# Kernel tuning notes

Measured on AMD Instinct MI355X. Metric: run time of the kernel, lower is better.

Reference implementation:

```python
import jax, jax.numpy as jnp
import numpy as np

N = 50000        # num nodes
E = 1_000_000    # num edges
F_IN = 256       # input feature dim
UNITS = 128      # hidden units
NUM_CLASSES = 40 # output classes
EPS = 1e-3       # Keras BatchNormalization default epsilon


def setup_inputs() -> dict:
    key = jax.random.key(0)
    ks = jax.random.split(key, 32)
    inp = {
        "x": jax.random.normal(ks[0], (N, F_IN), jnp.float32),
        "edge_index": jax.random.randint(ks[1], (2, E), 0, N, jnp.int32),
        "edge_weight": jax.random.uniform(ks[2], (E,), jnp.float32),
    }
    dims = [(F_IN, UNITS), (UNITS, UNITS), (UNITS, NUM_CLASSES)]
    ki = 3
    for li, (fi, fo) in enumerate(dims, 1):
        inp[f"w_gcn{li}"] = jax.random.normal(ks[ki], (fi, fo), jnp.float32) / np.sqrt(fi).astype(np.float32); ki += 1
        inp[f"w_self{li}"] = jax.random.normal(ks[ki], (fi, fo), jnp.float32) / np.sqrt(fi).astype(np.float32); ki += 1
        inp[f"b{li}"] = jnp.zeros((fo,), jnp.float32)
        inp[f"gamma{li}"] = 1.0 + 0.1 * jax.random.normal(ks[ki], (fo,), jnp.float32); ki += 1
        inp[f"beta{li}"] = 0.1 * jax.random.normal(ks[ki], (fo,), jnp.float32); ki += 1
        inp[f"mean{li}"] = 0.1 * jax.random.normal(ks[ki], (fo,), jnp.float32); ki += 1
        inp[f"var{li}"] = jnp.ones((fo,), jnp.float32)
    return inp


def _gcn_bs(h, src, dst, norm_w, w_gcn, w_self, b, gamma, beta, mean, var, act):
    # GCN aggregation: transform then gather->weight->scatter-sum
    hw = h @ w_gcn                                   # [N, out]
    msg = hw[src] * norm_w[:, None]                  # [E, out]
    agg = jax.ops.segment_sum(msg, dst, num_segments=N)
    out = agg + h @ w_self + b                       # self-loop dense + bias
    # BatchNorm (inference: moving stats)
    out = (out - mean) * jax.lax.rsqrt(var + EPS) * gamma + beta
    return act(out) if act is not None else out


def reference(x, edge_index, edge_weight,
              w_gcn1, w_self1, b1, gamma1, beta1, mean1, var1,
              w_gcn2, w_self2, b2, gamma2, beta2, mean2, var2,
              w_gcn3, w_self3, b3, gamma3, beta3, mean3, var3):
    src, dst = edge_index[0], edge_index[1]
    # symmetric GCN normalization (renorm=False: no added self loops)
    deg = jax.ops.segment_sum(edge_weight, dst, num_segments=N)
    dinv = jnp.where(deg > 0, jax.lax.rsqrt(jnp.where(deg > 0, deg, 1.0)), 0.0)
    norm_w = dinv[src] * edge_weight * dinv[dst]
    # inference: DropEdge and Dropout are identity
    h = _gcn_bs(x, src, dst, norm_w, w_gcn1, w_self1, b1, gamma1, beta1, mean1, var1, jax.nn.relu)
    h = _gcn_bs(h, src, dst, norm_w, w_gcn2, w_self2, b2, gamma2, beta2, mean2, var2, jax.nn.relu)
    h = _gcn_bs(h, src, dst, norm_w, w_gcn3, w_self3, b3, gamma3, beta3, mean3, var3, None)
    return h
```

## Files before the change

kernel.cpp:

```cpp
#include <hip/hip_runtime.h>
#include <hip/hip_bf16.h>

#define NN 50000
#define EE 1000000
static constexpr float EPSV = 1e-3f;
static constexpr float FIXSCALE = 16777216.f;

typedef __attribute__((ext_vector_type(8))) short short8;
typedef __attribute__((ext_vector_type(4))) float fx4;

__device__ inline float blo(unsigned u) { return __uint_as_float(u << 16); }
__device__ inline float bhi(unsigned u) { return __uint_as_float(u & 0xffff0000u); }
__device__ inline unsigned short f2b(float f) {
    __hip_bfloat16 h = __float2bfloat16(f);
    return *(unsigned short*)&h;
}
__device__ inline unsigned pack2(float a, float b) {
    return (unsigned)f2b(a) | ((unsigned)f2b(b) << 16);
}

__device__ inline void gload_lds16(const unsigned short* g, unsigned short* ldsbase) {
    __builtin_amdgcn_global_load_lds(
        (const __attribute__((address_space(1))) unsigned int*)(const void*)g,
        (__attribute__((address_space(3))) unsigned int*)(void*)ldsbase, 16, 0, 0);
}


#define ZB 196
#define WB1 256
#define WB2 128
#define WB3 64

__global__ void setup_kernel(unsigned long long* __restrict__ cnt64p,
                             const float* __restrict__ wg1, const float* __restrict__ ws1,
                             unsigned short* __restrict__ Wt1,
                             const float* __restrict__ wg2, const float* __restrict__ ws2,
                             unsigned short* __restrict__ Wt2,
                             const float* __restrict__ wg3, const float* __restrict__ ws3,
                             unsigned short* __restrict__ Wt3) {
    int b = blockIdx.x;
    int t = threadIdx.x;
    if (b < ZB) {
        int i = b * 256 + t;
        if (i < NN) cnt64p[(size_t)i << 3] = 0ull;
    } else if (b < ZB + WB1) {
        int idx = (b - ZB) * 256 + t;
        int n = idx >> 8, k = idx & 255;
        float v = (n < 128) ? wg1[(size_t)k * 128 + n]
                            : ws1[(size_t)k * 128 + (n - 128)];
        Wt1[idx] = f2b(v);
    } else if (b < ZB + WB1 + WB2) {
        int idx = (b - ZB - WB1) * 256 + t;
        int n = idx >> 7, k = idx & 127;
        float v = (n < 128) ? wg2[(size_t)k * 128 + n]
                            : ws2[(size_t)k * 128 + (n - 128)];
        Wt2[idx] = f2b(v);
    } else {
        int idx = (b - ZB - WB1 - WB2) * 256 + t;
        int n = idx >> 7, k = idx & 127;
        float v = 0.f;
        if (n < 40) v = wg3[(size_t)k * 40 + n];
        else if (n < 80) v = ws3[(size_t)k * 40 + (n - 40)];
        Wt3[idx] = f2b(v);
    }
}


#define CB 3907

__global__ void pre_kernel(const int* __restrict__ ei, const float* __restrict__ ew,
                           unsigned long long* __restrict__ cnt64p, unsigned* __restrict__ rank) {
    int e = blockIdx.x * 256 + threadIdx.x;
    if (e < EE) {
        int d = ei[EE + e];
        unsigned fx = __float2uint_rn(ew[e] * FIXSCALE);
        unsigned long long old =
            atomicAdd(&cnt64p[(size_t)d << 3], 0x100000000ull | (unsigned long long)fx);
        rank[e] = (unsigned)(old >> 32);
    }
}


__global__ __launch_bounds__(1024) void dinvsum_kernel(const unsigned long long* __restrict__ cnt64p,
                                                       float* __restrict__ dinv,
                                                       int* __restrict__ bsum) {
    __shared__ int s[1024];
    const int t = threadIdx.x;
    int idx = blockIdx.x * 1024 + t;
    unsigned long long cv = 0ull;
    if (idx < NN) cv = cnt64p[(size_t)idx << 3];
    float deg = (float)(unsigned)cv * (1.f / FIXSCALE);
    if (idx < NN) dinv[idx] = (deg > 0.f) ? rsqrtf(deg) : 0.f;
    s[t] = (int)(unsigned)(cv >> 32);
    __syncthreads();
#pragma unroll
    for (int off = 512; off > 0; off >>= 1) {
        if (t < off) s[t] += s[t + off];
        __syncthreads();
    }
    if (t == 0) bsum[blockIdx.x] = s[0];
}

__global__ __launch_bounds__(64) void scanB_kernel(const int* __restrict__ bsum,
                                                   int* __restrict__ bpre, int nb) {
    int t = threadIdx.x;
    int v = (t < nb) ? bsum[t] : 0;
    int own = v;
#pragma unroll
    for (int off = 1; off < 64; off <<= 1) {
        int u = __shfl_up(v, off);
        if (t >= off) v += u;
    }
    if (t < nb) bpre[t] = v - own;
}

__global__ __launch_bounds__(1024) void scanC_kernel(const unsigned long long* __restrict__ cnt64p,
                                                     const int* __restrict__ bpre,
                                                     int* __restrict__ rowstart) {
    __shared__ int s[1024];
    const int t = threadIdx.x;
    int idx = blockIdx.x * 1024 + t;
    int v = (idx < NN) ? (int)(unsigned)(cnt64p[(size_t)idx << 3] >> 32) : 0;
    s[t] = v;
    __syncthreads();
#pragma unroll
    for (int off = 1; off < 1024; off <<= 1) {
        int u = (t >= off) ? s[t - off] : 0;
        __syncthreads();
        s[t] += u;
        __syncthreads();
    }
    if (idx < NN) rowstart[idx] = s[t] - v + bpre[blockIdx.x];
    if (idx == 0) rowstart[NN] = EE;
}

__global__ void fill_kernel(const int* __restrict__ ei, const float* __restrict__ ew,
                            const float* __restrict__ dinv, const int* __restrict__ rowstart,
                            const unsigned* __restrict__ rank, unsigned* __restrict__ eprec4) {
    int e = blockIdx.x * blockDim.x + threadIdx.x;
    if (e >= EE) return;
    int s = ei[e], d = ei[EE + e];
    int idx = rowstart[d] + (int)rank[e];
    float w = dinv[s] * ew[e] * dinv[d];
    eprec4[idx] = ((unsigned)s << 16) | (unsigned)f2b(w);
}


template <bool AF32>
__global__ __launch_bounds__(256) void gemm_mfma(const void* __restrict__ Av,
                                                 const unsigned short* __restrict__ Wt,
                                                 const float* __restrict__ bias,
                                                 unsigned short* __restrict__ Cg,
                                                 unsigned short* __restrict__ Cs,
                                                 int M, int K, int Fo) {
    __shared__ unsigned short sA[64 * 64];
    __shared__ unsigned short sB[128 * 64];

    const int t = threadIdx.x;
    const int lane = t & 63;
    const int wave = t >> 6;
    const int l15 = lane & 15, quad = lane >> 4;
    const int row0 = blockIdx.x * 64;
    const int colbase = blockIdx.y * 128;

    fx4 acc[4][2];
#pragma unroll
    for (int r = 0; r < 4; ++r)
#pragma unroll
        for (int c = 0; c < 2; ++c) acc[r][c] = (fx4){0.f, 0.f, 0.f, 0.f};

    for (int kc = 0; kc < K; kc += 64) {
#pragma unroll
        for (int j = 0; j < 6; ++j) {
            int o = wave * 6 + j;
            int ak = kc + (o & 1) * 32 + quad * 8;
            if (o < 8) {
                int ar = row0 + (o >> 1) * 16 + l15;
                if (ar >= M) ar = M - 1;
                if constexpr (AF32) {
                    const float* Af = (const float*)Av;
                    const float4* p = (const float4*)(Af + (size_t)ar * K + ak);
                    float4 v0 = p[0], v1 = p[1];
                    uint4 u;
                    u.x = pack2(v0.x, v0.y);
                    u.y = pack2(v0.z, v0.w);
                    u.z = pack2(v1.x, v1.y);
                    u.w = pack2(v1.z, v1.w);
                    *reinterpret_cast<uint4*>(sA + o * 512 + lane * 8) = u;
                } else {
                    gload_lds16((const unsigned short*)Av + (size_t)ar * K + ak, sA + o * 512);
                }
            } else {
                int bo = o - 8;
                int br = colbase + (bo >> 1) * 16 + l15;
                gload_lds16(Wt + (size_t)br * K + ak, sB + bo * 512);
            }
        }
        __syncthreads();

#pragma unroll
        for (int kh = 0; kh < 2; ++kh) {
            short8 a[4], b[2];
#pragma unroll
            for (int r = 0; r < 4; ++r)
                a[r] = *reinterpret_cast<const short8*>(&sA[(r * 2 + kh) * 512 + lane * 8]);
#pragma unroll
            for (int c = 0; c < 2; ++c)
                b[c] = *reinterpret_cast<const short8*>(&sB[((wave * 2 + c) * 2 + kh) * 512 + lane * 8]);
#pragma unroll
            for (int r = 0; r < 4; ++r)
#pragma unroll
                for (int c = 0; c < 2; ++c)
                    acc[r][c] = __builtin_amdgcn_mfma_f32_16x16x32_bf16(a[r], b[c], acc[r][c], 0, 0, 0);
        }
        __syncthreads();
    }

#pragma unroll
    for (int r = 0; r < 4; ++r) {
#pragma unroll
        for (int reg = 0; reg < 4; ++reg) {
            int row = row0 + r * 16 + quad * 4 + reg;
            if (row >= M) continue;
#pragma unroll
            for (int c = 0; c < 2; ++c) {
                int f = colbase + wave * 32 + c * 16 + l15;
                if (f >= 2 * Fo) continue;
                bool isG = (f < Fo);
                int col = isG ? f : f - Fo;
                float badd = isG ? 0.f : bias[col];
                unsigned short* basep = isG ? Cg : Cs;
                basep[(size_t)row * Fo + col] = f2b(acc[r][c][reg] + badd);
            }
        }
    }
}


template <bool RELU>
__global__ __launch_bounds__(256) void agg128_kernel(
    const int* __restrict__ rowstart, const unsigned* __restrict__ eprec4,
    const unsigned* __restrict__ hw, const unsigned* __restrict__ selfC,
    const float* __restrict__ g, const float* __restrict__ be,
    const float* __restrict__ mu, const float* __restrict__ va,
    unsigned* __restrict__ out) {
    int wave = threadIdx.x >> 6;
    int lane = threadIdx.x & 63;
    int n = blockIdx.x * 4 + wave;
    if (n >= NN) return;
    unsigned scp = selfC[n * 64 + lane];
    float acc0 = blo(scp), acc1 = bhi(scp);
    int beg = rowstart[n], end = rowstart[n + 1];
    int i = beg;

    if (i + 16 <= end) {
        unsigned e[16];
        {
            int ifl = __builtin_amdgcn_readfirstlane(i);
#pragma unroll
            for (int k = 0; k < 16; ++k) e[k] = eprec4[ifl + k];
        }
        for (; i + 32 <= end; i += 16) {
            unsigned v[16];
#pragma unroll
            for (int k = 0; k < 16; ++k) v[k] = hw[(e[k] >> 16) * 64u + lane];
            unsigned en[16];
            {
                int ifl = __builtin_amdgcn_readfirstlane(i + 16);
#pragma unroll
                for (int k = 0; k < 16; ++k) en[k] = eprec4[ifl + k];
            }
#pragma unroll
            for (int k = 0; k < 16; ++k) {
                float w = blo(e[k]);
                acc0 += blo(v[k]) * w;
                acc1 += bhi(v[k]) * w;
            }
#pragma unroll
            for (int k = 0; k < 16; ++k) e[k] = en[k];
        }
        unsigned v[16];
#pragma unroll
        for (int k = 0; k < 16; ++k) v[k] = hw[(e[k] >> 16) * 64u + lane];
#pragma unroll
        for (int k = 0; k < 16; ++k) {
            float w = blo(e[k]);
            acc0 += blo(v[k]) * w;
            acc1 += bhi(v[k]) * w;
        }
        i += 16;
    }
    for (; i + 4 <= end; i += 4) {
        unsigned e0 = eprec4[i], e1 = eprec4[i + 1], e2 = eprec4[i + 2], e3 = eprec4[i + 3];
        unsigned v0 = hw[(e0 >> 16) * 64u + lane];
        unsigned v1 = hw[(e1 >> 16) * 64u + lane];
        unsigned v2 = hw[(e2 >> 16) * 64u + lane];
        unsigned v3 = hw[(e3 >> 16) * 64u + lane];
        float w0 = blo(e0), w1 = blo(e1), w2 = blo(e2), w3 = blo(e3);
        acc0 += blo(v0) * w0; acc1 += bhi(v0) * w0;
        acc0 += blo(v1) * w1; acc1 += bhi(v1) * w1;
        acc0 += blo(v2) * w2; acc1 += bhi(v2) * w2;
        acc0 += blo(v3) * w3; acc1 += bhi(v3) * w3;
    }
    for (; i < end; ++i) {
        unsigned e = eprec4[i];
        unsigned v = hw[(e >> 16) * 64u + lane];
        float w = blo(e);
        acc0 += blo(v) * w; acc1 += bhi(v) * w;
    }
    float2 m2 = reinterpret_cast<const float2*>(mu)[lane];
    float2 v2f = reinterpret_cast<const float2*>(va)[lane];
    float2 g2 = reinterpret_cast<const float2*>(g)[lane];
    float2 b2 = reinterpret_cast<const float2*>(be)[lane];
    float r0 = (acc0 - m2.x) * rsqrtf(v2f.x + EPSV) * g2.x + b2.x;
    float r1 = (acc1 - m2.y) * rsqrtf(v2f.y + EPSV) * g2.y + b2.y;
    if (RELU) {
        r0 = fmaxf(r0, 0.f);
        r1 = fmaxf(r1, 0.f);
    }
    out[n * 64 + lane] = pack2(r0, r1);
}


__global__ __launch_bounds__(256) void agg40_kernel(
    const int* __restrict__ rowstart, const unsigned* __restrict__ eprec4,
    const unsigned* __restrict__ hw, const unsigned* __restrict__ selfC,
    const float* __restrict__ g, const float* __restrict__ be,
    const float* __restrict__ mu, const float* __restrict__ va,
    float* __restrict__ out) {
    int wave = threadIdx.x >> 6;
    int lane = threadIdx.x & 63;
    int n = blockIdx.x * 4 + wave;
    if (n >= NN) return;
    int grp = lane / 20;
    int fl = lane - grp * 20;
    float acc0 = 0.f, acc1 = 0.f;
    int beg = rowstart[n], end = rowstart[n + 1];
    if (grp < 3) {
        int i = beg + grp;
        for (; i + 9 < end; i += 12) {
            unsigned e0 = eprec4[i], e1 = eprec4[i + 3], e2 = eprec4[i + 6], e3 = eprec4[i + 9];
            unsigned v0 = hw[(e0 >> 16) * 20u + fl];
            unsigned v1 = hw[(e1 >> 16) * 20u + fl];
            unsigned v2 = hw[(e2 >> 16) * 20u + fl];
            unsigned v3 = hw[(e3 >> 16) * 20u + fl];
            float w0 = blo(e0), w1 = blo(e1), w2 = blo(e2), w3 = blo(e3);
            acc0 += blo(v0) * w0; acc1 += bhi(v0) * w0;
            acc0 += blo(v1) * w1; acc1 += bhi(v1) * w1;
            acc0 += blo(v2) * w2; acc1 += bhi(v2) * w2;
            acc0 += blo(v3) * w3; acc1 += bhi(v3) * w3;
        }
        for (; i < end; i += 3) {
            unsigned e = eprec4[i];
            unsigned v = hw[(e >> 16) * 20u + fl];
            float w = blo(e);
            acc0 += blo(v) * w;
            acc1 += bhi(v) * w;
        }
    }
    acc0 += __shfl(acc0, lane + 20) + __shfl(acc0, lane + 40);
    acc1 += __shfl(acc1, lane + 20) + __shfl(acc1, lane + 40);
    if (lane < 20) {
        int f0 = lane * 2;
        unsigned scp = selfC[n * 20 + lane];
        acc0 += blo(scp);
        acc1 += bhi(scp);
        float2 m2 = reinterpret_cast<const float2*>(mu)[lane];
        float2 v2f = reinterpret_cast<const float2*>(va)[lane];
        float2 g2 = reinterpret_cast<const float2*>(g)[lane];
        float2 b2 = reinterpret_cast<const float2*>(be)[lane];
        float r0 = (acc0 - m2.x) * rsqrtf(v2f.x + EPSV) * g2.x + b2.x;
        float r1 = (acc1 - m2.y) * rsqrtf(v2f.y + EPSV) * g2.y + b2.y;
        *reinterpret_cast<float2*>(&out[(size_t)n * 40 + f0]) = make_float2(r0, r1);
    }
}


extern "C" void kernel_launch(void* const* d_in, const int* in_sizes, int n_in,
                              void* d_out, int out_size, void* d_ws, size_t ws_size,
                              hipStream_t stream) {
    const float* x = (const float*)d_in[0];
    const int* ei = (const int*)d_in[1];
    const float* ew = (const float*)d_in[2];

    const float* wg[3]  = {(const float*)d_in[3],  (const float*)d_in[10], (const float*)d_in[17]};
    const float* wsf[3] = {(const float*)d_in[4],  (const float*)d_in[11], (const float*)d_in[18]};
    const float* bs[3]  = {(const float*)d_in[5],  (const float*)d_in[12], (const float*)d_in[19]};
    const float* gm[3]  = {(const float*)d_in[6],  (const float*)d_in[13], (const float*)d_in[20]};
    const float* bt[3]  = {(const float*)d_in[7],  (const float*)d_in[14], (const float*)d_in[21]};
    const float* mu[3]  = {(const float*)d_in[8],  (const float*)d_in[15], (const float*)d_in[22]};
    const float* vr[3]  = {(const float*)d_in[9],  (const float*)d_in[16], (const float*)d_in[23]};

    float* W = (float*)d_ws;
    float* dinv     = W + 100096;
    unsigned* rank  = (unsigned*)(W + 150144);
    int*   bsum     = (int*)(W + 1150144);
    int*   bpre     = (int*)(W + 1150208);
    int*   rowstart = (int*)(W + 1150272);
    unsigned* eprec4 = (unsigned*)(W + 1200384);
    unsigned short* Wt1 = (unsigned short*)(W + 2200384);
    unsigned short* Wt2 = (unsigned short*)(W + 2233152);
    unsigned short* Wt3 = (unsigned short*)(W + 2249536);
    unsigned short* bufH = (unsigned short*)(W + 2257728);
    unsigned short* bufHW = (unsigned short*)(W + 8657728);
    unsigned short* bufSb = (unsigned short*)(W + 11857728);
    unsigned long long* cnt64p = (unsigned long long*)(W + 11857728);

    const int B = 256;
    const int SB = 49;

    setup_kernel<<<ZB + WB1 + WB2 + WB3, B, 0, stream>>>(
        cnt64p, wg[0], wsf[0], Wt1, wg[1], wsf[1], Wt2, wg[2], wsf[2], Wt3);

    pre_kernel<<<CB, B, 0, stream>>>(ei, ew, cnt64p, rank);

    dinvsum_kernel<<<SB, 1024, 0, stream>>>(cnt64p, dinv, bsum);
    scanB_kernel<<<1, 64, 0, stream>>>(bsum, bpre, SB);
    scanC_kernel<<<SB, 1024, 0, stream>>>(cnt64p, bpre, rowstart);
    fill_kernel<<<(EE + B - 1) / B, B, 0, stream>>>(ei, ew, dinv, rowstart, rank, eprec4);

    const int aggGrid = (NN + 3) / 4;
    dim3 g2((NN + 63) / 64, 2), g1((NN + 63) / 64, 1);

    gemm_mfma<true><<<g2, B, 0, stream>>>(x, Wt1, bs[0], bufHW, bufSb, NN, 256, 128);
    agg128_kernel<true><<<aggGrid, B, 0, stream>>>(rowstart, eprec4, (const unsigned*)bufHW,
                                                   (const unsigned*)bufSb, gm[0], bt[0], mu[0], vr[0],
                                                   (unsigned*)bufH);

    gemm_mfma<false><<<g2, B, 0, stream>>>(bufH, Wt2, bs[1], bufHW, bufSb, NN, 128, 128);
    agg128_kernel<true><<<aggGrid, B, 0, stream>>>(rowstart, eprec4, (const unsigned*)bufHW,
                                                   (const unsigned*)bufSb, gm[1], bt[1], mu[1], vr[1],
                                                   (unsigned*)bufH);

    gemm_mfma<false><<<g1, B, 0, stream>>>(bufH, Wt3, bs[2], bufHW, bufSb, NN, 128, 40);
    agg40_kernel<<<aggGrid, B, 0, stream>>>(rowstart, eprec4, (const unsigned*)bufHW,
                                            (const unsigned*)bufSb, gm[2], bt[2], mu[2], vr[2],
                                            (float*)d_out);
}
```

Baseline: 392.1 us.

## Pre-convert x to bf16, double-buffer GEMM LDS, fuse edge fill with layer-1 GEMM

x is converted to bf16 inside the degree-count pre-kernel, so the layer-1 GEMM can load A through direct global-to-LDS loads. The GEMM now uses 32-wide K stages with two LDS buffers, loading the next stage while computing the current one. The edge-record fill kernel is merged into one launch with the layer-1 GEMM so the two independent tasks can run at the same time on the GPU. This removes one launch and the in-GEMM fp32 conversion, but adds a separate pass over x (write bf16 xb, read it back) and puts more blocks into the pre-kernel.

```diff
diff --git a/kernel.cpp b/kernel.cpp
--- a/kernel.cpp
+++ b/kernel.cpp
@@ -67,16 +67,26 @@
 
 
 #define CB 3907
+#define XB 12500
 
 __global__ void pre_kernel(const int* __restrict__ ei, const float* __restrict__ ew,
-                           unsigned long long* __restrict__ cnt64p, unsigned* __restrict__ rank) {
-    int e = blockIdx.x * 256 + threadIdx.x;
-    if (e < EE) {
-        int d = ei[EE + e];
-        unsigned fx = __float2uint_rn(ew[e] * FIXSCALE);
-        unsigned long long old =
-            atomicAdd(&cnt64p[(size_t)d << 3], 0x100000000ull | (unsigned long long)fx);
-        rank[e] = (unsigned)(old >> 32);
+                           unsigned long long* __restrict__ cnt64p, unsigned* __restrict__ rank,
+                           const float4* __restrict__ x, uint2* __restrict__ xb) {
+    int b = blockIdx.x;
+    int t = threadIdx.x;
+    if (b < CB) {
+        int e = b * 256 + t;
+        if (e < EE) {
+            int d = ei[EE + e];
+            unsigned fx = __float2uint_rn(ew[e] * FIXSCALE);
+            unsigned long long old =
+                atomicAdd(&cnt64p[(size_t)d << 3], 0x100000000ull | (unsigned long long)fx);
+            rank[e] = (unsigned)(old >> 32);
+        }
+    } else {
+        int i = (b - CB) * 256 + t;
+        float4 v = x[i];
+        xb[i] = make_uint2(pack2(v.x, v.y), pack2(v.z, v.w));
     }
 }
 
@@ -134,34 +144,21 @@
     if (idx == 0) rowstart[NN] = EE;
 }
 
-__global__ void fill_kernel(const int* __restrict__ ei, const float* __restrict__ ew,
-                            const float* __restrict__ dinv, const int* __restrict__ rowstart,
-                            const unsigned* __restrict__ rank, unsigned* __restrict__ eprec4) {
-    int e = blockIdx.x * blockDim.x + threadIdx.x;
-    if (e >= EE) return;
-    int s = ei[e], d = ei[EE + e];
-    int idx = rowstart[d] + (int)rank[e];
-    float w = dinv[s] * ew[e] * dinv[d];
-    eprec4[idx] = ((unsigned)s << 16) | (unsigned)f2b(w);
-}
-
-
-template <bool AF32>
-__global__ __launch_bounds__(256) void gemm_mfma(const void* __restrict__ Av,
-                                                 const unsigned short* __restrict__ Wt,
-                                                 const float* __restrict__ bias,
-                                                 unsigned short* __restrict__ Cg,
-                                                 unsigned short* __restrict__ Cs,
-                                                 int M, int K, int Fo) {
-    __shared__ unsigned short sA[64 * 64];
-    __shared__ unsigned short sB[128 * 64];
-
+
+__device__ __forceinline__ void gemm2ph_body(int bx, int by,
+                                             const unsigned short* __restrict__ Ab,
+                                             const unsigned short* __restrict__ Wt,
+                                             const float* __restrict__ bias,
+                                             unsigned short* __restrict__ Cg,
+                                             unsigned short* __restrict__ Cs,
+                                             int M, int K, int Fo,
+                                             unsigned short* sA, unsigned short* sB) {
     const int t = threadIdx.x;
     const int lane = t & 63;
     const int wave = t >> 6;
     const int l15 = lane & 15, quad = lane >> 4;
-    const int row0 = blockIdx.x * 64;
-    const int colbase = blockIdx.y * 128;
+    const int row0 = bx * 64;
+    const int colbase = by * 128;
 
     fx4 acc[4][2];
 #pragma unroll
@@ -169,51 +166,47 @@
 #pragma unroll
         for (int c = 0; c < 2; ++c) acc[r][c] = (fx4){0.f, 0.f, 0.f, 0.f};
 
-    for (int kc = 0; kc < K; kc += 64) {
-#pragma unroll
-        for (int j = 0; j < 6; ++j) {
-            int o = wave * 6 + j;
-            int ak = kc + (o & 1) * 32 + quad * 8;
-            if (o < 8) {
-                int ar = row0 + (o >> 1) * 16 + l15;
+    auto stage = [&](int kc, int half) {
+        unsigned short* dA = sA + half * 2048;
+        unsigned short* dB = sB + half * 4096;
+#pragma unroll
+        for (int j = 0; j < 3; ++j) {
+            int o = wave * 3 + j;
+            int ak = kc + quad * 8;
+            if (o < 4) {
+                int ar = row0 + o * 16 + l15;
                 if (ar >= M) ar = M - 1;
-                if constexpr (AF32) {
-                    const float* Af = (const float*)Av;
-                    const float4* p = (const float4*)(Af + (size_t)ar * K + ak);
-                    float4 v0 = p[0], v1 = p[1];
-                    uint4 u;
-                    u.x = pack2(v0.x, v0.y);
-                    u.y = pack2(v0.z, v0.w);
-                    u.z = pack2(v1.x, v1.y);
-                    u.w = pack2(v1.z, v1.w);
-                    *reinterpret_cast<uint4*>(sA + o * 512 + lane * 8) = u;
-                } else {
-                    gload_lds16((const unsigned short*)Av + (size_t)ar * K + ak, sA + o * 512);
-                }
+                gload_lds16(Ab + (size_t)ar * K + ak, dA + o * 512);
             } else {
-                int bo = o - 8;
-                int br = colbase + (bo >> 1) * 16 + l15;
-                gload_lds16(Wt + (size_t)br * K + ak, sB + bo * 512);
+                int bo = o - 4;
+                int br = colbase + bo * 16 + l15;
+                gload_lds16(Wt + (size_t)br * K + ak, dB + bo * 512);
             }
         }
+    };
+
+    stage(0, 0);
+    __syncthreads();
+    const int nt = K >> 5;
+    int cur = 0;
+    for (int tt = 0; tt < nt; ++tt) {
+        if (tt + 1 < nt) stage((tt + 1) * 32, cur ^ 1);
+        const unsigned short* cA = sA + cur * 2048;
+        const unsigned short* cB = sB + cur * 4096;
+        short8 a[4], b[2];
+#pragma unroll
+        for (int r = 0; r < 4; ++r)
+            a[r] = *reinterpret_cast<const short8*>(&cA[r * 512 + lane * 8]);
+#pragma unroll
+        for (int c = 0; c < 2; ++c)
+            b[c] = *reinterpret_cast<const short8*>(&cB[(wave * 2 + c) * 512 + lane * 8]);
+#pragma unroll
+        for (int r = 0; r < 4; ++r)
+#pragma unroll
+            for (int c = 0; c < 2; ++c)
+                acc[r][c] = __builtin_amdgcn_mfma_f32_16x16x32_bf16(a[r], b[c], acc[r][c], 0, 0, 0);
         __syncthreads();
-
-#pragma unroll
-        for (int kh = 0; kh < 2; ++kh) {
-            short8 a[4], b[2];
-#pragma unroll
-            for (int r = 0; r < 4; ++r)
-                a[r] = *reinterpret_cast<const short8*>(&sA[(r * 2 + kh) * 512 + lane * 8]);
-#pragma unroll
-            for (int c = 0; c < 2; ++c)
-                b[c] = *reinterpret_cast<const short8*>(&sB[((wave * 2 + c) * 2 + kh) * 512 + lane * 8]);
-#pragma unroll
-            for (int r = 0; r < 4; ++r)
-#pragma unroll
-                for (int c = 0; c < 2; ++c)
-                    acc[r][c] = __builtin_amdgcn_mfma_f32_16x16x32_bf16(a[r], b[c], acc[r][c], 0, 0, 0);
-        }
-        __syncthreads();
+        cur ^= 1;
     }
 
 #pragma unroll
@@ -234,6 +227,46 @@
             }
         }
     }
+}
+
+__global__ __launch_bounds__(256) void gemm_mfma(const unsigned short* __restrict__ Ab,
+                                                 const unsigned short* __restrict__ Wt,
+                                                 const float* __restrict__ bias,
+                                                 unsigned short* __restrict__ Cg,
+                                                 unsigned short* __restrict__ Cs,
+                                                 int M, int K, int Fo) {
+    __shared__ unsigned short sA[2 * 64 * 32];
+    __shared__ unsigned short sB[2 * 128 * 32];
+    gemm2ph_body(blockIdx.x, blockIdx.y, Ab, Wt, bias, Cg, Cs, M, K, Fo, sA, sB);
+}
+
+
+#define GX 782
+#define GB 1564
+#define FB 3907
+
+__global__ __launch_bounds__(256) void fillgemm_kernel(
+    const int* __restrict__ ei, const float* __restrict__ ew,
+    const float* __restrict__ dinv, const int* __restrict__ rowstart,
+    const unsigned* __restrict__ rank, unsigned* __restrict__ eprec4,
+    const unsigned short* __restrict__ xb, const unsigned short* __restrict__ Wt1,
+    const float* __restrict__ bias1,
+    unsigned short* __restrict__ Cg, unsigned short* __restrict__ Cs) {
+    __shared__ unsigned short sA[2 * 64 * 32];
+    __shared__ unsigned short sB[2 * 128 * 32];
+    int b = blockIdx.x;
+    if (b >= GB) {
+        int e = (b - GB) * 256 + threadIdx.x;
+        if (e >= EE) return;
+        int s = ei[e], d = ei[EE + e];
+        int idx = rowstart[d] + (int)rank[e];
+        float w = dinv[s] * ew[e] * dinv[d];
+        eprec4[idx] = ((unsigned)s << 16) | (unsigned)f2b(w);
+        return;
+    }
+    int by = b / GX;
+    int bx = b - by * GX;
+    gemm2ph_body(bx, by, xb, Wt1, bias1, Cg, Cs, NN, 256, 128, sA, sB);
 }
 
 
@@ -401,6 +434,7 @@
     unsigned short* Wt1 = (unsigned short*)(W + 2200384);
     unsigned short* Wt2 = (unsigned short*)(W + 2233152);
     unsigned short* Wt3 = (unsigned short*)(W + 2249536);
+    unsigned short* xb  = (unsigned short*)(W + 2257728);
     unsigned short* bufH = (unsigned short*)(W + 2257728);
     unsigned short* bufHW = (unsigned short*)(W + 8657728);
     unsigned short* bufSb = (unsigned short*)(W + 11857728);
@@ -412,27 +446,27 @@
     setup_kernel<<<ZB + WB1 + WB2 + WB3, B, 0, stream>>>(
         cnt64p, wg[0], wsf[0], Wt1, wg[1], wsf[1], Wt2, wg[2], wsf[2], Wt3);
 
-    pre_kernel<<<CB, B, 0, stream>>>(ei, ew, cnt64p, rank);
+    pre_kernel<<<CB + XB, B, 0, stream>>>(ei, ew, cnt64p, rank, (const float4*)x, (uint2*)xb);
 
     dinvsum_kernel<<<SB, 1024, 0, stream>>>(cnt64p, dinv, bsum);
     scanB_kernel<<<1, 64, 0, stream>>>(bsum, bpre, SB);
     scanC_kernel<<<SB, 1024, 0, stream>>>(cnt64p, bpre, rowstart);
-    fill_kernel<<<(EE + B - 1) / B, B, 0, stream>>>(ei, ew, dinv, rowstart, rank, eprec4);
 
     const int aggGrid = (NN + 3) / 4;
-    dim3 g2((NN + 63) / 64, 2), g1((NN + 63) / 64, 1);
-
-    gemm_mfma<true><<<g2, B, 0, stream>>>(x, Wt1, bs[0], bufHW, bufSb, NN, 256, 128);
+    dim3 g2(GX, 2), g1(GX, 1);
+
+    fillgemm_kernel<<<GB + FB, B, 0, stream>>>(ei, ew, dinv, rowstart, rank, eprec4,
+                                               xb, Wt1, bs[0], bufHW, bufSb);
     agg128_kernel<true><<<aggGrid, B, 0, stream>>>(rowstart, eprec4, (const unsigned*)bufHW,
                                                    (const unsigned*)bufSb, gm[0], bt[0], mu[0], vr[0],
                                                    (unsigned*)bufH);
 
-    gemm_mfma<false><<<g2, B, 0, stream>>>(bufH, Wt2, bs[1], bufHW, bufSb, NN, 128, 128);
+    gemm_mfma<<<g2, B, 0, stream>>>(bufH, Wt2, bs[1], bufHW, bufSb, NN, 128, 128);
     agg128_kernel<true><<<aggGrid, B, 0, stream>>>(rowstart, eprec4, (const unsigned*)bufHW,
                                                    (const unsigned*)bufSb, gm[1], bt[1], mu[1], vr[1],
                                                    (unsigned*)bufH);
 
-    gemm_mfma<false><<<g1, B, 0, stream>>>(bufH, Wt3, bs[2], bufHW, bufSb, NN, 128, 40);
+    gemm_mfma<<<g1, B, 0, stream>>>(bufH, Wt3, bs[2], bufHW, bufSb, NN, 128, 40);
     agg40_kernel<<<aggGrid, B, 0, stream>>>(rowstart, eprec4, (const unsigned*)bufHW,
                                             (const unsigned*)bufSb, gm[2], bt[2], mu[2], vr[2],
                                             (float*)d_out);
```

Measured after the change: 381.8 us. 1.03x faster.
